# Optimization experiments

Hardware: AMD Instinct MI355X
Metric: run time of the kernel (lower is better)

Reference implementation:

```python
import jax, jax.numpy as jnp
import numpy as np
import math

L = 6      # num transformer layers
D = 128    # hidden_dim
H = 8      # heads
C = D // H # per-head dim (concat -> H*C == hidden_dim so residual add works)
F = 9      # node_features
OUT = 3    # output_dim
B, S, NN = 2, 128, 64
N = B * S * NN
E = 262144


def setup_inputs() -> dict:
    key = jax.random.key(0)
    ks = jax.random.split(key, 16)
    sc = 0.02
    g = lambda k, shp: jax.random.normal(k, shp, jnp.float32) * sc

    x = jax.random.normal(ks[0], (N, F), jnp.float32)
    edge_index = jax.random.randint(ks[1], (2, E), 0, N, dtype=jnp.int32)

    # sinusoidal positional encoding buffer [S, D]
    pos = np.arange(S, dtype=np.float32)[:, None]
    div = np.exp(np.arange(0, D, 2, dtype=np.float32) * (-math.log(10000.0) / D))
    pe = np.zeros((S, D), np.float32)
    pe[:, 0::2] = np.sin(pos * div)
    pe[:, 1::2] = np.cos(pos * div)

    return dict(
        x=x, edge_index=edge_index, pe=jnp.asarray(pe),
        Win=g(ks[2], (F, D)), bin_=jnp.zeros((D,), jnp.float32),
        Wq=g(ks[3], (L, D, D)), bq=jnp.zeros((L, D), jnp.float32),
        Wk=g(ks[4], (L, D, D)), bk=jnp.zeros((L, D), jnp.float32),
        Wv=g(ks[5], (L, D, D)), bv=jnp.zeros((L, D), jnp.float32),
        Ws=g(ks[6], (L, D, D)), bs=jnp.zeros((L, D), jnp.float32),
        Wb=g(ks[7], (L, 3 * D, 1)), bb=jnp.zeros((L, 1), jnp.float32),
        ln_g=jnp.ones((L, D), jnp.float32), ln_b=jnp.zeros((L, D), jnp.float32),
        Wo1=g(ks[8], (D, D // 2)), bo1=jnp.zeros((D // 2,), jnp.float32),
        Wo2=g(ks[9], (D // 2, OUT)), bo2=jnp.zeros((OUT,), jnp.float32),
        batch_size=B, seq_len=S, num_nodes=NN,
    )


def _layer_norm(x, g, b, eps=1e-5):
    mu = x.mean(-1, keepdims=True)
    var = ((x - mu) ** 2).mean(-1, keepdims=True)
    return (x - mu) / jnp.sqrt(var + eps) * g + b


def _transformer_conv(h, src, dst, Wq, bq, Wk, bk, Wv, bv, Ws, bs, Wb, bb):
    # PyG TransformerConv (beta=True, concat): edge gather -> per-head dot scores
    # -> scatter-softmax over incoming edges per dst node -> scatter-add aggregate.
    n = h.shape[0]
    q = (h @ Wq + bq).reshape(n, H, C)
    k = (h @ Wk + bk).reshape(n, H, C)
    v = (h @ Wv + bv).reshape(n, H, C)
    scores = jnp.einsum('ehc,ehc->eh', q[dst], k[src]) / math.sqrt(C)  # [E,H]
    m = jax.ops.segment_max(scores, dst, num_segments=n)               # [N,H]
    ex = jnp.exp(scores - jax.lax.stop_gradient(m)[dst])
    denom = jax.ops.segment_sum(ex, dst, num_segments=n)
    alpha = ex / (denom[dst] + 1e-16)                                  # [E,H]
    msg = (v[src] * alpha[:, :, None]).reshape(-1, H * C)              # [E,D]
    agg = jax.ops.segment_sum(msg, dst, num_segments=n)                # [N,D]
    xr = h @ Ws + bs                                                   # skip branch
    beta = jax.nn.sigmoid(jnp.concatenate([agg, xr, agg - xr], -1) @ Wb + bb)
    return beta * xr + (1.0 - beta) * agg


def reference(x, edge_index, pe, Win, bin_, Wq, bq, Wk, bk, Wv, bv, Ws, bs,
              Wb, bb, ln_g, ln_b, Wo1, bo1, Wo2, bo2,
              batch_size, seq_len, num_nodes):
    src, dst = edge_index[0], edge_index[1]
    d = Win.shape[1]
    h = x @ Win + bin_
    # add temporal positional encoding per timestep
    h = (h.reshape(batch_size, seq_len, num_nodes, d)
         + pe[:seq_len][None, :, None, :]).reshape(-1, d)
    for i in range(Wq.shape[0]):
        hn = _transformer_conv(h, src, dst, Wq[i], bq[i], Wk[i], bk[i],
                               Wv[i], bv[i], Ws[i], bs[i], Wb[i], bb[i])
        h = _layer_norm(h + hn, ln_g[i], ln_b[i])
    return jax.nn.relu(h @ Wo1 + bo1) @ Wo2 + bo2
```

## Files before the change

### kernel.cpp

```cpp
#include <hip/hip_runtime.h>

#define NNODES 16384
#define EDGES  262144
#define DH     128
#define NH     8
#define CH     16
#define NL     6
#define SEQ    128
#define NNPG   64

typedef short bf16x8 __attribute__((ext_vector_type(8)));
typedef float f32x4 __attribute__((ext_vector_type(4)));
typedef float f32x2 __attribute__((ext_vector_type(2)));

static __device__ __forceinline__ unsigned short f2bf(float f) {
  unsigned u = __float_as_uint(f);
  u += 0x7FFFu + ((u >> 16) & 1u);
  return (unsigned short)(u >> 16);
}
static __device__ __forceinline__ float bfl(unsigned u) { return __uint_as_float(u << 16); }
static __device__ __forceinline__ float bfh(unsigned u) { return __uint_as_float(u & 0xffff0000u); }

__global__ __launch_bounds__(128) void k_input(const float* __restrict__ x,
    const float* __restrict__ Win, const float* __restrict__ bin,
    const float* __restrict__ pe, float* __restrict__ h,
    unsigned short* __restrict__ hb) {
  const int n = blockIdx.x, d = threadIdx.x;
  __shared__ float xs[9];
  if (d < 9) xs[d] = x[n * 9 + d];
  __syncthreads();
  float acc = bin[d];
#pragma unroll
  for (int f = 0; f < 9; ++f) acc = fmaf(xs[f], Win[f * DH + d], acc);
  const float val = acc + pe[((n / NNPG) % SEQ) * DH + d];
  h[n * DH + d] = val;
  hb[n * DH + d] = f2bf(val);
}

__global__ __launch_bounds__(256) void k_count(const int* __restrict__ ei,
                                               int* __restrict__ cnt) {
  const int e = blockIdx.x * 256 + threadIdx.x;
  atomicAdd(&cnt[ei[EDGES + e]], 1);
}

__global__ __launch_bounds__(1024) void k_scan(int* __restrict__ cnt,
                                               int* __restrict__ row_start) {
  __shared__ int part[1024];
  const int t = threadIdx.x;
  int loc[16];
  int s = 0;
  const int base = t * 16;
#pragma unroll
  for (int i = 0; i < 16; ++i) { loc[i] = cnt[base + i]; s += loc[i]; }
  part[t] = s;
  __syncthreads();
  for (int off = 1; off < 1024; off <<= 1) {
    int add = (t >= off) ? part[t - off] : 0;
    __syncthreads();
    part[t] += add;
    __syncthreads();
  }
  int run = (t == 0) ? 0 : part[t - 1];
#pragma unroll
  for (int i = 0; i < 16; ++i) {
    row_start[base + i] = run;
    run += loc[i];
    cnt[base + i] = 0;
  }
  if (t == 0) row_start[NNODES] = EDGES;
}

__global__ __launch_bounds__(256) void k_fill(const int* __restrict__ ei,
    const int* __restrict__ row_start, int* __restrict__ cursor,
    int* __restrict__ csr_src) {
  const int e = blockIdx.x * 256 + threadIdx.x;
  const int d = ei[EDGES + e];
  csr_src[row_start[d] + atomicAdd(&cursor[d], 1)] = ei[e];
}

__global__ __launch_bounds__(64) void k_wconv(const float* __restrict__ Wq,
    const float* __restrict__ Wk, const float* __restrict__ Wv,
    const float* __restrict__ Ws, unsigned short* __restrict__ Wf) {
  const int bid = blockIdx.x;
  const int layer = bid >> 7, rem = bid & 127;
  const int mat = rem >> 5, tile = rem & 31;
  const int nt = tile >> 2, kt = tile & 3;
  const int lane = threadIdx.x;
  const float* W = ((mat == 0) ? Wq : (mat == 1) ? Wk : (mat == 2) ? Wv : Ws)
                   + layer * DH * DH;
  const int n = nt * 16 + (lane & 15);
  const int k0 = kt * 32 + (lane >> 4) * 8;
  unsigned pk[4];
#pragma unroll
  for (int jj = 0; jj < 4; ++jj) {
    const unsigned lo = f2bf(W[(k0 + 2 * jj) * DH + n]);
    const unsigned hi = f2bf(W[(k0 + 2 * jj + 1) * DH + n]);
    pk[jj] = lo | (hi << 16);
  }
  uint4 o = {pk[0], pk[1], pk[2], pk[3]};
  *(uint4*)&Wf[(((layer * 4 + mat) * 32 + tile) * 64 + lane) * 8] = o;
}

__global__ __launch_bounds__(256) void k_gemm(const unsigned short* __restrict__ hb,
    const unsigned short* __restrict__ Wf,
    const float* __restrict__ bq, const float* __restrict__ bk,
    const float* __restrict__ bv, const float* __restrict__ bs,
    unsigned short* __restrict__ qb, unsigned char* __restrict__ kv8,
    float* __restrict__ xr) {
  const int mt = blockIdx.x;
  const int wv = threadIdx.x >> 6, lane = threadIdx.x & 63;
  const int g = blockIdx.y * 4 + wv;
  const int mat = g >> 1, nbase = (g & 1) * 64;
  const unsigned short* Wm = Wf + mat * 16384;
  const float* bias = (mat == 0) ? bq : (mat == 1) ? bk : (mat == 2) ? bv : bs;
  const int m0 = lane & 15, quad = lane >> 4;
  const int nt0 = (g & 1) * 4;

  const f32x4 z = {0.f, 0.f, 0.f, 0.f};
  f32x4 acc[2][4] = {{z, z, z, z}, {z, z, z, z}};
#pragma unroll
  for (int kt = 0; kt < 4; ++kt) {
    const bf16x8 a0 = *(const bf16x8*)&hb[(mt * 32 + m0) * DH + kt * 32 + quad * 8];
    const bf16x8 a1 = *(const bf16x8*)&hb[(mt * 32 + 16 + m0) * DH + kt * 32 + quad * 8];
#pragma unroll
    for (int j = 0; j < 4; ++j) {
      const bf16x8 b = *(const bf16x8*)&Wm[(((nt0 + j) * 4 + kt) * 64 + lane) * 8];
      acc[0][j] = __builtin_amdgcn_mfma_f32_16x16x32_bf16(a0, b, acc[0][j], 0, 0, 0);
      acc[1][j] = __builtin_amdgcn_mfma_f32_16x16x32_bf16(a1, b, acc[1][j], 0, 0, 0);
    }
  }
  const int kvoff = (mat == 1) ? 0 : 128;
#pragma unroll
  for (int half = 0; half < 2; ++half) {
#pragma unroll
    for (int j = 0; j < 4; ++j) {
      const int col = nbase + j * 16 + m0;
      const float bvv = bias[col];
#pragma unroll
      for (int r = 0; r < 4; ++r) {
        const float val = acc[half][j][r] + bvv;
        const int row = mt * 32 + half * 16 + quad * 4 + r;
        if (mat == 0) {
          qb[row * DH + col] = f2bf(val);
        } else if (mat == 3) {
          xr[row * DH + col] = val;
        } else {
          const float nbv = __shfl_xor(val, 1);
          if ((lane & 1) == 0) {
            const int pk = __builtin_amdgcn_cvt_pk_fp8_f32(val, nbv, 0, false);
            *(unsigned short*)&kv8[row * 256 + kvoff + col] = (unsigned short)pk;
          }
        }
      }
    }
  }
}

__device__ __forceinline__ void load16bf(const unsigned short* __restrict__ p, float* r) {
  const uint4 a = *(const uint4*)p;
  const uint4 b = *(const uint4*)(p + 8);
  r[0] = bfl(a.x); r[1] = bfh(a.x); r[2] = bfl(a.y); r[3] = bfh(a.y);
  r[4] = bfl(a.z); r[5] = bfh(a.z); r[6] = bfl(a.w); r[7] = bfh(a.w);
  r[8] = bfl(b.x); r[9] = bfh(b.x); r[10] = bfl(b.y); r[11] = bfh(b.y);
  r[12] = bfl(b.z); r[13] = bfh(b.z); r[14] = bfl(b.w); r[15] = bfh(b.w);
}

__device__ __forceinline__ void decode16f8(const uint4 u, float* r) {
  f32x2 t;
  t = __builtin_amdgcn_cvt_pk_f32_fp8(u.x, false); r[0] = t[0]; r[1] = t[1];
  t = __builtin_amdgcn_cvt_pk_f32_fp8(u.x, true);  r[2] = t[0]; r[3] = t[1];
  t = __builtin_amdgcn_cvt_pk_f32_fp8(u.y, false); r[4] = t[0]; r[5] = t[1];
  t = __builtin_amdgcn_cvt_pk_f32_fp8(u.y, true);  r[6] = t[0]; r[7] = t[1];
  t = __builtin_amdgcn_cvt_pk_f32_fp8(u.z, false); r[8] = t[0]; r[9] = t[1];
  t = __builtin_amdgcn_cvt_pk_f32_fp8(u.z, true);  r[10] = t[0]; r[11] = t[1];
  t = __builtin_amdgcn_cvt_pk_f32_fp8(u.w, false); r[12] = t[0]; r[13] = t[1];
  t = __builtin_amdgcn_cvt_pk_f32_fp8(u.w, true);  r[14] = t[0]; r[15] = t[1];
}

__device__ __forceinline__ void edge_acc_m(const uint4 ku, const uint4 vu, bool valid,
    const float* __restrict__ qr, float* __restrict__ acc, float& denom) {
  float kr[16], vr[16];
  decode16f8(ku, kr);
  float dot = 0.f;
#pragma unroll
  for (int c = 0; c < 16; ++c) dot = fmaf(qr[c], kr[c], dot);
  const float ex = valid ? __expf(dot * 0.25f) : 0.f;
  denom += ex;
  decode16f8(vu, vr);
#pragma unroll
  for (int c = 0; c < 16; ++c) acc[c] = fmaf(ex, vr[c], acc[c]);
}

__global__ __launch_bounds__(256, 4) void k_attn_epi(const unsigned short* __restrict__ qb,
    const unsigned char* __restrict__ kv8,
    const int* __restrict__ row_start, const int* __restrict__ csr_src,
    float* __restrict__ h, unsigned short* __restrict__ hb,
    const float* __restrict__ xr,
    const float* __restrict__ Wb, const float* __restrict__ bb,
    const float* __restrict__ ln_g, const float* __restrict__ ln_b) {
  const int wv = threadIdx.x >> 6, lane = threadIdx.x & 63;
  const int n = blockIdx.x * 4 + wv;
  const int es = lane >> 3, hd = lane & 7;
  const int beg = row_start[n], end = row_start[n + 1];
  const int j0 = beg + es;
  int idx[4];
#pragma unroll
  for (int t = 0; t < 4; ++t) {
    const int jt = j0 + 8 * t;
    idx[t] = (jt < end) ? csr_src[jt] : -1;
  }
  float qr[16];
  load16bf(&qb[n * DH + hd * CH], qr);
  uint4 kf[4], vf[4];
#pragma unroll
  for (int t = 0; t < 4; ++t) {
    const int s = (idx[t] >= 0) ? idx[t] : 0;
    const unsigned char* base = &kv8[s * 256 + hd * CH];
    kf[t] = *(const uint4*)base;
    vf[t] = *(const uint4*)(base + 128);
  }
  float acc[16] = {};
  float denom = 0.f;
#pragma unroll
  for (int t = 0; t < 4; ++t)
    edge_acc_m(kf[t], vf[t], idx[t] >= 0, qr, acc, denom);
  for (int j = j0 + 32; j < end; j += 8) {
    const int s = csr_src[j];
    const unsigned char* base = &kv8[s * 256 + hd * CH];
    const uint4 ku = *(const uint4*)base;
    const uint4 vu = *(const uint4*)(base + 128);
    edge_acc_m(ku, vu, true, qr, acc, denom);
  }
#pragma unroll
  for (int off = 8; off <= 32; off <<= 1) {
    denom += __shfl_xor(denom, off);
#pragma unroll
    for (int c = 0; c < 16; ++c) acc[c] += __shfl_xor(acc[c], off);
  }
  const float inv = 1.f / (denom + 1e-16f);
  float o0 = 0.f, o1 = 0.f;
#pragma unroll
  for (int c = 0; c < 8; ++c) {
    if (es == c) { o0 = acc[2 * c]; o1 = acc[2 * c + 1]; }
  }
  const int d0 = hd * CH + es * 2;
  const float ax = o0 * inv, ay = o1 * inv;
  const float2 r = *(const float2*)&xr[n * DH + d0];
  const float2 w0 = *(const float2*)&Wb[d0];
  const float2 w1 = *(const float2*)&Wb[DH + d0];
  const float2 w2 = *(const float2*)&Wb[2 * DH + d0];
  float p = ax * w0.x + ay * w0.y + r.x * w1.x + r.y * w1.y
          + (ax - r.x) * w2.x + (ay - r.y) * w2.y;
#pragma unroll
  for (int off = 1; off <= 32; off <<= 1) p += __shfl_xor(p, off);
  const float beta = 1.f / (1.f + __expf(-(p + bb[0])));
  const float2 hv = *(const float2*)&h[n * DH + d0];
  const float t0 = hv.x + beta * r.x + (1.f - beta) * ax;
  const float t1 = hv.y + beta * r.y + (1.f - beta) * ay;
  float sum = t0 + t1, sq = t0 * t0 + t1 * t1;
#pragma unroll
  for (int off = 1; off <= 32; off <<= 1) {
    sum += __shfl_xor(sum, off);
    sq  += __shfl_xor(sq, off);
  }
  const float mu = sum * (1.f / DH);
  const float rinv = rsqrtf(sq * (1.f / DH) - mu * mu + 1e-5f);
  const float2 g = *(const float2*)&ln_g[d0];
  const float2 b = *(const float2*)&ln_b[d0];
  float2 o = {(t0 - mu) * rinv * g.x + b.x, (t1 - mu) * rinv * g.y + b.y};
  *(float2*)&h[n * DH + d0] = o;
  const unsigned lo = f2bf(o.x), hi = f2bf(o.y);
  *(unsigned*)&hb[n * DH + d0] = lo | (hi << 16);
}

__global__ __launch_bounds__(256) void k_final(const float* __restrict__ h,
    const float* __restrict__ Wo1, const float* __restrict__ bo1,
    const float* __restrict__ Wo2, const float* __restrict__ bo2,
    float* __restrict__ out) {
  __shared__ float hs[4][DH];
  const int lane = threadIdx.x & 63, wid = threadIdx.x >> 6;
  const int n = blockIdx.x * 4 + wid;
  const float2 hv = *(const float2*)&h[n * DH + lane * 2];
  hs[wid][lane * 2] = hv.x;
  hs[wid][lane * 2 + 1] = hv.y;
  __syncthreads();
  float m = bo1[lane];
#pragma unroll 16
  for (int d = 0; d < DH; ++d) m = fmaf(hs[wid][d], Wo1[d * 64 + lane], m);
  m = fmaxf(m, 0.f);
  float o0 = m * Wo2[lane * 3 + 0];
  float o1 = m * Wo2[lane * 3 + 1];
  float o2 = m * Wo2[lane * 3 + 2];
#pragma unroll
  for (int off = 32; off; off >>= 1) {
    o0 += __shfl_xor(o0, off);
    o1 += __shfl_xor(o1, off);
    o2 += __shfl_xor(o2, off);
  }
  if (lane == 0) {
    out[n * 3 + 0] = o0 + bo2[0];
    out[n * 3 + 1] = o1 + bo2[1];
    out[n * 3 + 2] = o2 + bo2[2];
  }
}

extern "C" void kernel_launch(void* const* d_in, const int* in_sizes, int n_in,
                              void* d_out, int out_size, void* d_ws, size_t ws_size,
                              hipStream_t stream) {
  const float* x   = (const float*)d_in[0];
  const int*   ei  = (const int*)d_in[1];
  const float* pe  = (const float*)d_in[2];
  const float* Win = (const float*)d_in[3];
  const float* bin = (const float*)d_in[4];
  const float* Wq  = (const float*)d_in[5];
  const float* bq  = (const float*)d_in[6];
  const float* Wk  = (const float*)d_in[7];
  const float* bk  = (const float*)d_in[8];
  const float* Wv  = (const float*)d_in[9];
  const float* bv  = (const float*)d_in[10];
  const float* Wsk = (const float*)d_in[11];
  const float* bs  = (const float*)d_in[12];
  const float* Wb  = (const float*)d_in[13];
  const float* bb  = (const float*)d_in[14];
  const float* lng = (const float*)d_in[15];
  const float* lnb = (const float*)d_in[16];
  const float* Wo1 = (const float*)d_in[17];
  const float* bo1 = (const float*)d_in[18];
  const float* Wo2 = (const float*)d_in[19];
  const float* bo2 = (const float*)d_in[20];

  const size_t NU = (size_t)NNODES * DH;
  char* base = (char*)d_ws;
  float* h   = (float*)base;                  base += NU * 4;
  float* xr  = (float*)base;                  base += NU * 4;
  unsigned short* hb = (unsigned short*)base; base += NU * 2;
  unsigned short* qb = (unsigned short*)base; base += NU * 2;
  unsigned char* kv8 = (unsigned char*)base;  base += NU * 2;
  unsigned short* Wf = (unsigned short*)base; base += (size_t)NL * 4 * 16384 * 2;
  int* row_start = (int*)base;                base += (NNODES + 1) * 4;
  int* cnt       = (int*)base;                base += NNODES * 4;
  int* csr_src   = (int*)base;

  (void)hipMemsetAsync(cnt, 0, NNODES * sizeof(int), stream);
  k_count<<<EDGES / 256, 256, 0, stream>>>(ei, cnt);
  k_scan<<<1, 1024, 0, stream>>>(cnt, row_start);
  k_fill<<<EDGES / 256, 256, 0, stream>>>(ei, row_start, cnt, csr_src);
  k_wconv<<<NL * 128, 64, 0, stream>>>(Wq, Wk, Wv, Wsk, Wf);
  k_input<<<NNODES, 128, 0, stream>>>(x, Win, bin, pe, h, hb);
  for (int l = 0; l < NL; ++l) {
    k_gemm<<<dim3(NNODES / 32, 2), 256, 0, stream>>>(
        hb, Wf + (size_t)l * 4 * 16384,
        bq + l * DH, bk + l * DH, bv + l * DH, bs + l * DH, qb, kv8, xr);
    k_attn_epi<<<NNODES / 4, 256, 0, stream>>>(qb, kv8, row_start, csr_src,
                                               h, hb, xr, Wb + l * 3 * DH, bb + l,
                                               lng + l * DH, lnb + l * DH);
  }
  k_final<<<NNODES / 4, 256, 0, stream>>>(h, Wo1, bo1, Wo2, bo2, (float*)d_out);
}
```

Baseline: 386.3 us.

## Drop fp32 hidden and skip buffers, keep them in bf16; enlarge GEMM row tile

```diff
diff --git a/kernel.cpp b/kernel.cpp
--- a/kernel.cpp
+++ b/kernel.cpp
@@ -23,8 +23,7 @@
 
 __global__ __launch_bounds__(128) void k_input(const float* __restrict__ x,
     const float* __restrict__ Win, const float* __restrict__ bin,
-    const float* __restrict__ pe, float* __restrict__ h,
-    unsigned short* __restrict__ hb) {
+    const float* __restrict__ pe, unsigned short* __restrict__ hb) {
   const int n = blockIdx.x, d = threadIdx.x;
   __shared__ float xs[9];
   if (d < 9) xs[d] = x[n * 9 + d];
@@ -32,9 +31,7 @@
   float acc = bin[d];
 #pragma unroll
   for (int f = 0; f < 9; ++f) acc = fmaf(xs[f], Win[f * DH + d], acc);
-  const float val = acc + pe[((n / NNPG) % SEQ) * DH + d];
-  h[n * DH + d] = val;
-  hb[n * DH + d] = f2bf(val);
+  hb[n * DH + d] = f2bf(acc + pe[((n / NNPG) % SEQ) * DH + d]);
 }
 
 __global__ __launch_bounds__(256) void k_count(const int* __restrict__ ei,
@@ -106,7 +103,7 @@
     const float* __restrict__ bq, const float* __restrict__ bk,
     const float* __restrict__ bv, const float* __restrict__ bs,
     unsigned short* __restrict__ qb, unsigned char* __restrict__ kv8,
-    float* __restrict__ xr) {
+    unsigned short* __restrict__ xrb) {
   const int mt = blockIdx.x;
   const int wv = threadIdx.x >> 6, lane = threadIdx.x & 63;
   const int g = blockIdx.y * 4 + wv;
@@ -117,33 +114,36 @@
   const int nt0 = (g & 1) * 4;
 
   const f32x4 z = {0.f, 0.f, 0.f, 0.f};
-  f32x4 acc[2][4] = {{z, z, z, z}, {z, z, z, z}};
+  f32x4 acc[4][4] = {{z, z, z, z}, {z, z, z, z}, {z, z, z, z}, {z, z, z, z}};
 #pragma unroll
   for (int kt = 0; kt < 4; ++kt) {
-    const bf16x8 a0 = *(const bf16x8*)&hb[(mt * 32 + m0) * DH + kt * 32 + quad * 8];
-    const bf16x8 a1 = *(const bf16x8*)&hb[(mt * 32 + 16 + m0) * DH + kt * 32 + quad * 8];
+    bf16x8 a[4];
+#pragma unroll
+    for (int q = 0; q < 4; ++q)
+      a[q] = *(const bf16x8*)&hb[(mt * 64 + q * 16 + m0) * DH + kt * 32 + quad * 8];
 #pragma unroll
     for (int j = 0; j < 4; ++j) {
       const bf16x8 b = *(const bf16x8*)&Wm[(((nt0 + j) * 4 + kt) * 64 + lane) * 8];
-      acc[0][j] = __builtin_amdgcn_mfma_f32_16x16x32_bf16(a0, b, acc[0][j], 0, 0, 0);
-      acc[1][j] = __builtin_amdgcn_mfma_f32_16x16x32_bf16(a1, b, acc[1][j], 0, 0, 0);
+#pragma unroll
+      for (int q = 0; q < 4; ++q)
+        acc[q][j] = __builtin_amdgcn_mfma_f32_16x16x32_bf16(a[q], b, acc[q][j], 0, 0, 0);
     }
   }
   const int kvoff = (mat == 1) ? 0 : 128;
 #pragma unroll
-  for (int half = 0; half < 2; ++half) {
+  for (int q = 0; q < 4; ++q) {
 #pragma unroll
     for (int j = 0; j < 4; ++j) {
       const int col = nbase + j * 16 + m0;
       const float bvv = bias[col];
 #pragma unroll
       for (int r = 0; r < 4; ++r) {
-        const float val = acc[half][j][r] + bvv;
-        const int row = mt * 32 + half * 16 + quad * 4 + r;
+        const float val = acc[q][j][r] + bvv;
+        const int row = mt * 64 + q * 16 + quad * 4 + r;
         if (mat == 0) {
           qb[row * DH + col] = f2bf(val);
         } else if (mat == 3) {
-          xr[row * DH + col] = val;
+          xrb[row * DH + col] = f2bf(val);
         } else {
           const float nbv = __shfl_xor(val, 1);
           if ((lane & 1) == 0) {
@@ -194,8 +194,7 @@
 __global__ __launch_bounds__(256, 4) void k_attn_epi(const unsigned short* __restrict__ qb,
     const unsigned char* __restrict__ kv8,
     const int* __restrict__ row_start, const int* __restrict__ csr_src,
-    float* __restrict__ h, unsigned short* __restrict__ hb,
-    const float* __restrict__ xr,
+    unsigned short* __restrict__ hb, const unsigned short* __restrict__ xrb,
     const float* __restrict__ Wb, const float* __restrict__ bb,
     const float* __restrict__ ln_g, const float* __restrict__ ln_b) {
   const int wv = threadIdx.x >> 6, lane = threadIdx.x & 63;
@@ -245,18 +244,19 @@
   }
   const int d0 = hd * CH + es * 2;
   const float ax = o0 * inv, ay = o1 * inv;
-  const float2 r = *(const float2*)&xr[n * DH + d0];
+  const unsigned xu = *(const unsigned*)&xrb[n * DH + d0];
+  const float rx = bfl(xu), ry = bfh(xu);
   const float2 w0 = *(const float2*)&Wb[d0];
   const float2 w1 = *(const float2*)&Wb[DH + d0];
   const float2 w2 = *(const float2*)&Wb[2 * DH + d0];
-  float p = ax * w0.x + ay * w0.y + r.x * w1.x + r.y * w1.y
-          + (ax - r.x) * w2.x + (ay - r.y) * w2.y;
+  float p = ax * w0.x + ay * w0.y + rx * w1.x + ry * w1.y
+          + (ax - rx) * w2.x + (ay - ry) * w2.y;
 #pragma unroll
   for (int off = 1; off <= 32; off <<= 1) p += __shfl_xor(p, off);
   const float beta = 1.f / (1.f + __expf(-(p + bb[0])));
-  const float2 hv = *(const float2*)&h[n * DH + d0];
-  const float t0 = hv.x + beta * r.x + (1.f - beta) * ax;
-  const float t1 = hv.y + beta * r.y + (1.f - beta) * ay;
+  const unsigned hu = *(const unsigned*)&hb[n * DH + d0];
+  const float t0 = bfl(hu) + beta * rx + (1.f - beta) * ax;
+  const float t1 = bfh(hu) + beta * ry + (1.f - beta) * ay;
   float sum = t0 + t1, sq = t0 * t0 + t1 * t1;
 #pragma unroll
   for (int off = 1; off <= 32; off <<= 1) {
@@ -267,22 +267,22 @@
   const float rinv = rsqrtf(sq * (1.f / DH) - mu * mu + 1e-5f);
   const float2 g = *(const float2*)&ln_g[d0];
   const float2 b = *(const float2*)&ln_b[d0];
-  float2 o = {(t0 - mu) * rinv * g.x + b.x, (t1 - mu) * rinv * g.y + b.y};
-  *(float2*)&h[n * DH + d0] = o;
-  const unsigned lo = f2bf(o.x), hi = f2bf(o.y);
+  const float ox = (t0 - mu) * rinv * g.x + b.x;
+  const float oy = (t1 - mu) * rinv * g.y + b.y;
+  const unsigned lo = f2bf(ox), hi = f2bf(oy);
   *(unsigned*)&hb[n * DH + d0] = lo | (hi << 16);
 }
 
-__global__ __launch_bounds__(256) void k_final(const float* __restrict__ h,
+__global__ __launch_bounds__(256) void k_final(const unsigned short* __restrict__ hb,
     const float* __restrict__ Wo1, const float* __restrict__ bo1,
     const float* __restrict__ Wo2, const float* __restrict__ bo2,
     float* __restrict__ out) {
   __shared__ float hs[4][DH];
   const int lane = threadIdx.x & 63, wid = threadIdx.x >> 6;
   const int n = blockIdx.x * 4 + wid;
-  const float2 hv = *(const float2*)&h[n * DH + lane * 2];
-  hs[wid][lane * 2] = hv.x;
-  hs[wid][lane * 2 + 1] = hv.y;
+  const unsigned hu = *(const unsigned*)&hb[n * DH + lane * 2];
+  hs[wid][lane * 2] = bfl(hu);
+  hs[wid][lane * 2 + 1] = bfh(hu);
   __syncthreads();
   float m = bo1[lane];
 #pragma unroll 16
@@ -331,14 +331,13 @@
 
   const size_t NU = (size_t)NNODES * DH;
   char* base = (char*)d_ws;
-  float* h   = (float*)base;                  base += NU * 4;
-  float* xr  = (float*)base;                  base += NU * 4;
-  unsigned short* hb = (unsigned short*)base; base += NU * 2;
-  unsigned short* qb = (unsigned short*)base; base += NU * 2;
-  unsigned char* kv8 = (unsigned char*)base;  base += NU * 2;
-  unsigned short* Wf = (unsigned short*)base; base += (size_t)NL * 4 * 16384 * 2;
-  int* row_start = (int*)base;                base += (NNODES + 1) * 4;
-  int* cnt       = (int*)base;                base += NNODES * 4;
+  unsigned short* hb  = (unsigned short*)base; base += NU * 2;
+  unsigned short* qb  = (unsigned short*)base; base += NU * 2;
+  unsigned short* xrb = (unsigned short*)base; base += NU * 2;
+  unsigned char*  kv8 = (unsigned char*)base;  base += NU * 2;
+  unsigned short* Wf  = (unsigned short*)base; base += (size_t)NL * 4 * 16384 * 2;
+  int* row_start = (int*)base;                 base += (NNODES + 1) * 4;
+  int* cnt       = (int*)base;                 base += NNODES * 4;
   int* csr_src   = (int*)base;
 
   (void)hipMemsetAsync(cnt, 0, NNODES * sizeof(int), stream);
@@ -346,14 +345,14 @@
   k_scan<<<1, 1024, 0, stream>>>(cnt, row_start);
   k_fill<<<EDGES / 256, 256, 0, stream>>>(ei, row_start, cnt, csr_src);
   k_wconv<<<NL * 128, 64, 0, stream>>>(Wq, Wk, Wv, Wsk, Wf);
-  k_input<<<NNODES, 128, 0, stream>>>(x, Win, bin, pe, h, hb);
+  k_input<<<NNODES, 128, 0, stream>>>(x, Win, bin, pe, hb);
   for (int l = 0; l < NL; ++l) {
-    k_gemm<<<dim3(NNODES / 32, 2), 256, 0, stream>>>(
+    k_gemm<<<dim3(NNODES / 64, 2), 256, 0, stream>>>(
         hb, Wf + (size_t)l * 4 * 16384,
-        bq + l * DH, bk + l * DH, bv + l * DH, bs + l * DH, qb, kv8, xr);
+        bq + l * DH, bk + l * DH, bv + l * DH, bs + l * DH, qb, kv8, xrb);
     k_attn_epi<<<NNODES / 4, 256, 0, stream>>>(qb, kv8, row_start, csr_src,
-                                               h, hb, xr, Wb + l * 3 * DH, bb + l,
+                                               hb, xrb, Wb + l * 3 * DH, bb + l,
                                                lng + l * DH, lnb + l * DH);
   }
-  k_final<<<NNODES / 4, 256, 0, stream>>>(h, Wo1, bo1, Wo2, bo2, (float*)d_out);
-}
+  k_final<<<NNODES / 4, 256, 0, stream>>>(hb, Wo1, bo1, Wo2, bo2, (float*)d_out);
+}
```

Measured after the change: 401.7 us. +4.0%, slower.
